# Kernel optimization log

Hardware: AMD Instinct MI355X
Metric: run time of the kernel (lower is better)

The kernel has to match this reference:

```python
import jax, jax.numpy as jnp
from jax import lax
import numpy as np

N = 200000
H = 64          # h
C = 2 * H       # 2h feature channels
L = 128         # voxel grid side
KV = 125        # 5^3 kernel volume
KEEP = KV // 2 + 1  # 63 offsets kept by mask type 'B' (incl. center)


def _build_kernel_map(coords):
    # coords: [N,3] int voxel coords, unique. Returns nidx [KEEP, N] int32, -1 if no neighbor.
    keys = (coords[:, 0].astype(np.int64) * L + coords[:, 1]) * L + coords[:, 2]
    order = np.argsort(keys)
    skeys = keys[order]
    nidx = np.full((KEEP, N), -1, dtype=np.int32)
    for k in range(KEEP):
        dx, dy, dz = k // 25 - 2, (k // 5) % 5 - 2, k % 5 - 2
        nc = coords + np.array([dx, dy, dz])
        inb = np.all((nc >= 0) & (nc < L), axis=1)
        qk = (nc[:, 0].astype(np.int64) * L + nc[:, 1]) * L + nc[:, 2]
        pos = np.searchsorted(skeys, qk)
        posc = np.minimum(pos, N - 1)
        found = inb & (skeys[posc] == qk)
        nidx[k] = np.where(found, order[posc].astype(np.int32), -1)
    return nidx


def setup_inputs() -> dict:
    key = jax.random.key(0)
    k1, k2, k3, k4, k5 = jax.random.split(key, 5)
    rng = np.random.default_rng(0)
    flat = rng.choice(L ** 3, size=N, replace=False)
    coords = np.stack(np.unravel_index(flat, (L, L, L)), axis=1).astype(np.int32)
    nidx = jnp.asarray(_build_kernel_map(coords))
    s = 0.05
    return {
        "x_feats": jax.random.normal(k1, (N, C), jnp.float32),
        "y_feats": jax.random.normal(k2, (N, C), jnp.float32),
        "Wa": jax.random.normal(k3, (C, H), jnp.float32) * s,
        "Wb": jax.random.normal(k4, (KV, H, H), jnp.float32) * s,
        "Wc": jax.random.normal(k5, (H, C), jnp.float32) * s,
        "nidx": nidx,
    }


def reference(x_feats, y_feats, Wa, Wb, Wc, nidx):
    # mask type 'B': zero kernel offsets >= KV//2 + 1
    mask = (jnp.arange(KV) < KEEP)[:, None, None].astype(Wb.dtype)
    Wb_kept = (Wb * mask)[:KEEP]  # [KEEP, H, H]; remaining offsets contribute 0

    def block(f):
        f = jax.nn.elu(f)
        f = f @ Wa                      # 1x1 conv 2h->h
        f = jax.nn.elu(f)
        # masked sparse 5^3 conv: gather-GEMM-accumulate over kernel offsets
        def body(acc, kw):
            idx, W = kw                 # idx [N], W [H,H]
            g = jnp.where((idx >= 0)[:, None], f[jnp.maximum(idx, 0)], 0.0)
            return acc + g @ W, None
        acc0 = jnp.zeros((f.shape[0], H), f.dtype)
        f, _ = lax.scan(body, acc0, (nidx, Wb_kept))
        f = jax.nn.elu(f)
        return f @ Wc                   # 1x1 conv h->2h

    out = x_feats + y_feats
    return x_feats + block(out)
```

## Files before the change

### kernel.cpp

```cpp
#include <hip/hip_runtime.h>
#include <cmath>

#define N_PTS 200000
#define HD 64
#define CD 128
#define KEEP 63

typedef __bf16 bf16;
typedef __bf16 bf16x4 __attribute__((ext_vector_type(4)));
typedef __bf16 bf16x8 __attribute__((ext_vector_type(8)));
typedef float f32x4 __attribute__((ext_vector_type(4)));
typedef float f32x16 __attribute__((ext_vector_type(16)));

__device__ __forceinline__ float elu_f(float v) {
    return v > 0.f ? v : __expf(v) - 1.f;
}

__global__ __launch_bounds__(256) void k_prep(const float* __restrict__ Wb,
                                              const float* __restrict__ Wc,
                                              const float* __restrict__ Wa,
                                              bf16* __restrict__ WbT,
                                              bf16* __restrict__ WcT,
                                              bf16* __restrict__ WaT,
                                              bf16* __restrict__ zp) {
    int idx = blockIdx.x * 256 + threadIdx.x;
    if (idx < KEEP * HD * HD) {
        int k = idx >> 12;
        int rem = idx & 4095;
        int o = rem >> 6, i = rem & 63;
        int dst = ((i >> 4) * 2 + (o >> 5)) * 512 +
                  (((i >> 3) & 1) * 32 + (o & 31)) * 8 + (i & 7);
        WbT[(k << 12) + dst] = (bf16)Wb[(k * HD + i) * HD + o];
        return;
    }
    int e = idx - KEEP * HD * HD;
    if (e < CD * HD) {
        int c = e >> 6, h = e & 63;
        WcT[e] = (bf16)Wc[h * CD + c];
        return;
    }
    e -= CD * HD;
    if (e < HD * CD) {
        int o = e >> 7, c = e & 127;
        int dst = ((c >> 4) * 2 + (o >> 5)) * 512 +
                  (((c >> 3) & 1) * 32 + (o & 31)) * 8 + (c & 7);
        WaT[dst] = (bf16)Wa[c * HD + o];
        return;
    }
    e -= HD * CD;
    if (e < 64) zp[e] = (bf16)0.f;
}

__global__ __launch_bounds__(256, 4) void k_stage1(const float* __restrict__ x,
                                                   const float* __restrict__ y,
                                                   const bf16* __restrict__ WaT,
                                                   bf16* __restrict__ f) {
    __shared__ bf16 pbuf[4][32 * 64];
    int tid = threadIdx.x;
    int wave = tid >> 6;
    int lane = tid & 63;
    int l31 = lane & 31;
    int half = lane >> 5;
    int pbase_w = blockIdx.x * 128 + wave * 32;
    int p = pbase_w + l31;
    int pc = p < N_PTS ? p : N_PTS - 1;

    const float* xr = x + (size_t)pc * CD;
    const float* yr = y + (size_t)pc * CD;

    f32x16 acc[2];
#pragma unroll
    for (int mt = 0; mt < 2; mt++)
#pragma unroll
        for (int r = 0; r < 16; r++) acc[mt][r] = 0.f;

    f32x4 xa[2], xb[2], ya[2], yb[2];
    {
        int c0 = half * 8;
        xa[0] = *(const f32x4*)(xr + c0);
        xb[0] = *(const f32x4*)(xr + c0 + 4);
        ya[0] = *(const f32x4*)(yr + c0);
        yb[0] = *(const f32x4*)(yr + c0 + 4);
    }
#pragma unroll
    for (int ks = 0; ks < 8; ks++) {
        int cur = ks & 1, nxt = cur ^ 1;
        bf16x8 a0 = *(const bf16x8*)(WaT + (ks * 2 + 0) * 512 + lane * 8);
        bf16x8 a1 = *(const bf16x8*)(WaT + (ks * 2 + 1) * 512 + lane * 8);
        __builtin_amdgcn_sched_barrier(0);
        if (ks < 7) {
            int c0 = half * 8 + (ks + 1) * 16;
            xa[nxt] = *(const f32x4*)(xr + c0);
            xb[nxt] = *(const f32x4*)(xr + c0 + 4);
            ya[nxt] = *(const f32x4*)(yr + c0);
            yb[nxt] = *(const f32x4*)(yr + c0 + 4);
        }
        bf16x8 bv;
#pragma unroll
        for (int jj = 0; jj < 4; jj++) {
            bv[jj]     = (bf16)elu_f(xa[cur][jj] + ya[cur][jj]);
            bv[4 + jj] = (bf16)elu_f(xb[cur][jj] + yb[cur][jj]);
        }
        acc[0] = __builtin_amdgcn_mfma_f32_32x32x16_bf16(a0, bv, acc[0], 0, 0, 0);
        acc[1] = __builtin_amdgcn_mfma_f32_32x32x16_bf16(a1, bv, acc[1], 0, 0, 0);
        __builtin_amdgcn_sched_barrier(0);
    }

    bf16* pb = pbuf[wave];
#pragma unroll
    for (int mt = 0; mt < 2; mt++) {
#pragma unroll
        for (int q = 0; q < 4; q++) {
            bf16x4 v;
#pragma unroll
            for (int jj = 0; jj < 4; jj++)
                v[jj] = (bf16)elu_f(acc[mt][q * 4 + jj]);
            int chunk = mt * 4 + q;
            *(bf16x4*)&pb[l31 * 64 + ((chunk ^ (l31 & 7)) * 8) + 4 * half] = v;
        }
    }
#pragma unroll
    for (int qq = 0; qq < 4; qq++) {
        int t = lane + 64 * qq;
        int row = t >> 3, ch = t & 7;
        int pos = ch ^ (row & 7);
        bf16x8 v = *(const bf16x8*)&pb[row * 64 + pos * 8];
        int pp = pbase_w + row;
        if (pp < N_PTS)
            *(bf16x8*)(f + (size_t)pp * HD + ch * 8) = v;
    }
}

struct BB { bf16x8 v[4]; };
struct AF { bf16x8 v[8]; };

__global__ __launch_bounds__(256, 2) void k_conv(const bf16* __restrict__ f,
                                                 const int* __restrict__ nidx,
                                                 const bf16* __restrict__ WbT,
                                                 const bf16* __restrict__ WcT,
                                                 const bf16* __restrict__ zp,
                                                 const float* __restrict__ x,
                                                 float* __restrict__ out) {
    __shared__ bf16 wcs[128 * 64];
    __shared__ bf16 pbuf[4 * 32 * 64];

    int tid = threadIdx.x;
    int wave = tid >> 6;
    int lane = tid & 63;
    int l31 = lane & 31;
    int half = lane >> 5;
    int pbase = blockIdx.x * 256 + wave * 64;
    int p0 = pbase + l31;
    int p1 = pbase + 32 + l31;

    f32x16 acc[2][2];
#pragma unroll
    for (int a = 0; a < 2; a++)
#pragma unroll
        for (int b = 0; b < 2; b++)
#pragma unroll
            for (int r = 0; r < 16; r++) acc[a][b][r] = 0.f;

#pragma unroll
    for (int L = tid; L < 1024; L += 256) {
        int c = L >> 3, ci = L & 7;
        bf16x8 v = *(const bf16x8*)&WcT[L * 8];
        *(bf16x8*)&wcs[c * 64 + ((ci ^ (c & 7)) * 8)] = v;
    }

    auto ldidx = [&](int k, int pp) -> int {
        return (k < KEEP && pp < N_PTS) ? nidx[(size_t)k * N_PTS + pp] : -1;
    };
    auto baddr = [&](int iv) -> const bf16* {
        return iv >= 0 ? f + (size_t)iv * HD + half * 8 : zp + half * 8;
    };
    auto gather = [&](BB& b, const bf16* a) {
#pragma unroll
        for (int ks = 0; ks < 4; ks++)
            b.v[ks] = *(const bf16x8*)(a + ks * 16);
    };
    auto loadA = [&](int k, AF& A) {
        const bf16* wk = WbT + ((size_t)k << 12);
#pragma unroll
        for (int fi = 0; fi < 8; fi++)
            A.v[fi] = *(const bf16x8*)(wk + fi * 512 + lane * 8);
    };
    auto mstep = [&](const AF& A, BB& q0, BB& q1) {
#pragma unroll
        for (int ks = 0; ks < 4; ks++) {
#pragma unroll
            for (int mt = 0; mt < 2; mt++) {
                acc[mt][0] = __builtin_amdgcn_mfma_f32_32x32x16_bf16(A.v[ks * 2 + mt], q0.v[ks], acc[mt][0], 0, 0, 0);
                acc[mt][1] = __builtin_amdgcn_mfma_f32_32x32x16_bf16(A.v[ks * 2 + mt], q1.v[ks], acc[mt][1], 0, 0, 0);
            }
        }
    };

    BB b0a, b0b, b1a, b1b, b2a, b2b;
    int i2a = ldidx(2, p0), i2b = ldidx(2, p1);
    int i0a = ldidx(3, p0), i0b = ldidx(3, p1);
    int i1a = ldidx(4, p0), i1b = ldidx(4, p1);
    {
        int ja = ldidx(0, p0), jb = ldidx(0, p1);
        int ka = ldidx(1, p0), kb = ldidx(1, p1);
        gather(b0a, baddr(ja)); gather(b0b, baddr(jb));
        gather(b1a, baddr(ka)); gather(b1b, baddr(kb));
    }

    AF Af;
    for (int j = 0; j < 20; j++) {
        int k = 3 * j;
        loadA(k, Af);
        __builtin_amdgcn_sched_barrier(0);
        gather(b2a, baddr(i2a)); gather(b2b, baddr(i2b));
        i2a = ldidx(k + 5, p0);  i2b = ldidx(k + 5, p1);
        mstep(Af, b0a, b0b);
        __builtin_amdgcn_sched_barrier(0);
        loadA(k + 1, Af);
        __builtin_amdgcn_sched_barrier(0);
        gather(b0a, baddr(i0a)); gather(b0b, baddr(i0b));
        i0a = ldidx(k + 6, p0);  i0b = ldidx(k + 6, p1);
        mstep(Af, b1a, b1b);
        __builtin_amdgcn_sched_barrier(0);
        loadA(k + 2, Af);
        __builtin_amdgcn_sched_barrier(0);
        gather(b1a, baddr(i1a)); gather(b1b, baddr(i1b));
        i1a = ldidx(k + 7, p0);  i1b = ldidx(k + 7, p1);
        mstep(Af, b2a, b2b);
        __builtin_amdgcn_sched_barrier(0);
    }
    loadA(60, Af);
    __builtin_amdgcn_sched_barrier(0);
    gather(b2a, baddr(i2a)); gather(b2b, baddr(i2b));
    mstep(Af, b0a, b0b);
    __builtin_amdgcn_sched_barrier(0);
    loadA(61, Af);
    __builtin_amdgcn_sched_barrier(0);
    mstep(Af, b1a, b1b);
    __builtin_amdgcn_sched_barrier(0);
    loadA(62, Af);
    __builtin_amdgcn_sched_barrier(0);
    mstep(Af, b2a, b2b);

    __syncthreads();

    bf16* pb = &pbuf[wave * 2048];
#pragma unroll
    for (int pt = 0; pt < 2; pt++) {
#pragma unroll
        for (int mt = 0; mt < 2; mt++) {
#pragma unroll
            for (int q = 0; q < 4; q++) {
                bf16x4 v;
#pragma unroll
                for (int jj = 0; jj < 4; jj++)
                    v[jj] = (bf16)elu_f(acc[mt][pt][q * 4 + jj]);
                int chunk = mt * 4 + q;
                *(bf16x4*)&pb[l31 * 64 + ((chunk ^ (l31 & 7)) * 8) + 4 * half] = v;
            }
        }
        bf16x8 pa[4];
#pragma unroll
        for (int ks = 0; ks < 4; ks++) {
            int ci = 2 * ks + half;
            pa[ks] = *(const bf16x8*)&pb[l31 * 64 + ((ci ^ (l31 & 7)) * 8)];
        }
#pragma unroll
        for (int ct = 0; ct < 4; ct++) {
            f32x16 o;
#pragma unroll
            for (int r = 0; r < 16; r++) o[r] = 0.f;
            int cc = ct * 32 + l31;
#pragma unroll
            for (int ks = 0; ks < 4; ks++) {
                int ci = 2 * ks + half;
                bf16x8 bw = *(const bf16x8*)&wcs[cc * 64 + ((ci ^ (cc & 7)) * 8)];
                o = __builtin_amdgcn_mfma_f32_32x32x16_bf16(pa[ks], bw, o, 0, 0, 0);
            }
            int prow_base = pbase + pt * 32 + 4 * half;
#pragma unroll
            for (int r = 0; r < 16; r++) {
                int prow = prow_base + (r & 3) + 8 * (r >> 2);
                if (prow < N_PTS) {
                    size_t off = (size_t)prow * CD + cc;
                    out[off] = x[off] + o[r];
                }
            }
        }
    }
}

extern "C" void kernel_launch(void* const* d_in, const int* in_sizes, int n_in,
                              void* d_out, int out_size, void* d_ws, size_t ws_size,
                              hipStream_t stream) {
    const float* x  = (const float*)d_in[0];
    const float* y  = (const float*)d_in[1];
    const float* Wa = (const float*)d_in[2];
    const float* Wb = (const float*)d_in[3];
    const float* Wc = (const float*)d_in[4];
    const int* nidx = (const int*)d_in[5];
    float* out = (float*)d_out;

    char* ws = (char*)d_ws;
    bf16* f   = (bf16*)ws;
    bf16* WbT = (bf16*)(ws + 25624576);
    bf16* WcT = (bf16*)(ws + 25624576 + 516096);
    bf16* WaT = (bf16*)(ws + 25624576 + 516096 + 16384);
    bf16* zp  = (bf16*)(ws + 25624576 + 516096 + 16384 + 16384);

    k_prep<<<1073, 256, 0, stream>>>(Wb, Wc, Wa, WbT, WcT, WaT, zp);
    k_stage1<<<1564, 256, 0, stream>>>(x, y, WaT, f);
    k_conv<<<782, 256, 0, stream>>>(f, nidx, WbT, WcT, zp, x, out);
}
```

Measured before the change: 551.8 us.

## Restructure sparse conv gather through per-wave LDS bounce with double-buffered weights

The conv kernel now gives each wave 32 points instead of 64. Neighbor rows are gathered with 8 lanes per row, so each 128-byte feature row is read contiguously. The gathered rows are staged in a swizzled per-wave LDS buffer and read back as MFMA operands. Weight fragments are double-buffered across kernel offsets, Wc is pre-laid-out in fragment order and read straight from global instead of LDS, and occupancy is raised to 4 blocks per CU. The aim is more coalesced gathers and better latency hiding, at the cost of reloading the weight fragments for every 32 points rather than every 64, plus extra LDS traffic. Stage1 prefetch is also deepened from 1 to 2 steps ahead.

```diff
diff --git a/kernel.cpp b/kernel.cpp
--- a/kernel.cpp
+++ b/kernel.cpp
@@ -20,7 +20,7 @@
                                               const float* __restrict__ Wc,
                                               const float* __restrict__ Wa,
                                               bf16* __restrict__ WbT,
-                                              bf16* __restrict__ WcT,
+                                              bf16* __restrict__ WcT2,
                                               bf16* __restrict__ WaT,
                                               bf16* __restrict__ zp) {
     int idx = blockIdx.x * 256 + threadIdx.x;
@@ -36,7 +36,9 @@
     int e = idx - KEEP * HD * HD;
     if (e < CD * HD) {
         int c = e >> 6, h = e & 63;
-        WcT[e] = (bf16)Wc[h * CD + c];
+        int dst = ((c >> 5) * 4 + (h >> 4)) * 512 +
+                  ((((h >> 3) & 1) * 32) + (c & 31)) * 8 + (h & 7);
+        WcT2[dst] = (bf16)Wc[h * CD + c];
         return;
     }
     e -= CD * HD;
@@ -74,22 +76,23 @@
 #pragma unroll
         for (int r = 0; r < 16; r++) acc[mt][r] = 0.f;
 
-    f32x4 xa[2], xb[2], ya[2], yb[2];
-    {
-        int c0 = half * 8;
-        xa[0] = *(const f32x4*)(xr + c0);
-        xb[0] = *(const f32x4*)(xr + c0 + 4);
-        ya[0] = *(const f32x4*)(yr + c0);
-        yb[0] = *(const f32x4*)(yr + c0 + 4);
+    f32x4 xa[3], xb[3], ya[3], yb[3];
+#pragma unroll
+    for (int pre = 0; pre < 2; pre++) {
+        int c0 = half * 8 + pre * 16;
+        xa[pre] = *(const f32x4*)(xr + c0);
+        xb[pre] = *(const f32x4*)(xr + c0 + 4);
+        ya[pre] = *(const f32x4*)(yr + c0);
+        yb[pre] = *(const f32x4*)(yr + c0 + 4);
     }
 #pragma unroll
     for (int ks = 0; ks < 8; ks++) {
-        int cur = ks & 1, nxt = cur ^ 1;
+        int cur = ks % 3, nxt = (ks + 2) % 3;
         bf16x8 a0 = *(const bf16x8*)(WaT + (ks * 2 + 0) * 512 + lane * 8);
         bf16x8 a1 = *(const bf16x8*)(WaT + (ks * 2 + 1) * 512 + lane * 8);
         __builtin_amdgcn_sched_barrier(0);
-        if (ks < 7) {
-            int c0 = half * 8 + (ks + 1) * 16;
+        if (ks < 6) {
+            int c0 = half * 8 + (ks + 2) * 16;
             xa[nxt] = *(const f32x4*)(xr + c0);
             xb[nxt] = *(const f32x4*)(xr + c0 + 4);
             ya[nxt] = *(const f32x4*)(yr + c0);
@@ -131,53 +134,53 @@
     }
 }
 
-struct BB { bf16x8 v[4]; };
+struct GR { bf16x8 v[4]; };
 struct AF { bf16x8 v[8]; };
 
-__global__ __launch_bounds__(256, 2) void k_conv(const bf16* __restrict__ f,
+__global__ __launch_bounds__(256, 4) void k_conv(const bf16* __restrict__ f,
                                                  const int* __restrict__ nidx,
                                                  const bf16* __restrict__ WbT,
-                                                 const bf16* __restrict__ WcT,
+                                                 const bf16* __restrict__ WcT2,
                                                  const bf16* __restrict__ zp,
                                                  const float* __restrict__ x,
                                                  float* __restrict__ out) {
-    __shared__ bf16 wcs[128 * 64];
-    __shared__ bf16 pbuf[4 * 32 * 64];
+    __shared__ bf16 bounce[4][32 * 64];
 
     int tid = threadIdx.x;
     int wave = tid >> 6;
     int lane = tid & 63;
     int l31 = lane & 31;
     int half = lane >> 5;
-    int pbase = blockIdx.x * 256 + wave * 64;
-    int p0 = pbase + l31;
-    int p1 = pbase + 32 + l31;
-
-    f32x16 acc[2][2];
-#pragma unroll
-    for (int a = 0; a < 2; a++)
-#pragma unroll
-        for (int b = 0; b < 2; b++)
-#pragma unroll
-            for (int r = 0; r < 16; r++) acc[a][b][r] = 0.f;
-
-#pragma unroll
-    for (int L = tid; L < 1024; L += 256) {
-        int c = L >> 3, ci = L & 7;
-        bf16x8 v = *(const bf16x8*)&WcT[L * 8];
-        *(bf16x8*)&wcs[c * 64 + ((ci ^ (c & 7)) * 8)] = v;
-    }
-
-    auto ldidx = [&](int k, int pp) -> int {
+    int g8 = lane >> 3;
+    int l7 = lane & 7;
+    int pbase = blockIdx.x * 128 + wave * 32;
+
+    bf16* pb = bounce[wave];
+
+    f32x16 acc[2];
+#pragma unroll
+    for (int mt = 0; mt < 2; mt++)
+#pragma unroll
+        for (int r = 0; r < 16; r++) acc[mt][r] = 0.f;
+
+    auto ldidx4 = [&](int k, int i) -> int {
+        int pp = pbase + i * 8 + g8;
         return (k < KEEP && pp < N_PTS) ? nidx[(size_t)k * N_PTS + pp] : -1;
     };
-    auto baddr = [&](int iv) -> const bf16* {
-        return iv >= 0 ? f + (size_t)iv * HD + half * 8 : zp + half * 8;
-    };
-    auto gather = [&](BB& b, const bf16* a) {
-#pragma unroll
-        for (int ks = 0; ks < 4; ks++)
-            b.v[ks] = *(const bf16x8*)(a + ks * 16);
+    auto gaddr = [&](int iv) -> const bf16* {
+        return iv >= 0 ? f + (size_t)iv * HD + l7 * 8 : zp + l7 * 8;
+    };
+    auto gather4 = [&](GR& g, const int (&iv)[4]) {
+#pragma unroll
+        for (int i = 0; i < 4; i++)
+            g.v[i] = *(const bf16x8*)gaddr(iv[i]);
+    };
+    auto dswrite = [&](const GR& g) {
+#pragma unroll
+        for (int i = 0; i < 4; i++) {
+            int pp = i * 8 + g8;
+            *(bf16x8*)&pb[pp * 64 + ((l7 ^ g8) * 8)] = g.v[i];
+        }
     };
     auto loadA = [&](int k, AF& A) {
         const bf16* wk = WbT + ((size_t)k << 12);
@@ -185,106 +188,100 @@
         for (int fi = 0; fi < 8; fi++)
             A.v[fi] = *(const bf16x8*)(wk + fi * 512 + lane * 8);
     };
-    auto mstep = [&](const AF& A, BB& q0, BB& q1) {
+    auto mfma8 = [&](const AF& a) {
 #pragma unroll
         for (int ks = 0; ks < 4; ks++) {
-#pragma unroll
-            for (int mt = 0; mt < 2; mt++) {
-                acc[mt][0] = __builtin_amdgcn_mfma_f32_32x32x16_bf16(A.v[ks * 2 + mt], q0.v[ks], acc[mt][0], 0, 0, 0);
-                acc[mt][1] = __builtin_amdgcn_mfma_f32_32x32x16_bf16(A.v[ks * 2 + mt], q1.v[ks], acc[mt][1], 0, 0, 0);
-            }
-        }
-    };
-
-    BB b0a, b0b, b1a, b1b, b2a, b2b;
-    int i2a = ldidx(2, p0), i2b = ldidx(2, p1);
-    int i0a = ldidx(3, p0), i0b = ldidx(3, p1);
-    int i1a = ldidx(4, p0), i1b = ldidx(4, p1);
+            int ci = ks * 2 + half;
+            bf16x8 fb = *(const bf16x8*)&pb[l31 * 64 + ((ci ^ (l31 & 7)) * 8)];
+            acc[0] = __builtin_amdgcn_mfma_f32_32x32x16_bf16(a.v[ks * 2 + 0], fb, acc[0], 0, 0, 0);
+            acc[1] = __builtin_amdgcn_mfma_f32_32x32x16_bf16(a.v[ks * 2 + 1], fb, acc[1], 0, 0, 0);
+        }
+    };
+    auto substep = [&](int k, AF& Aload, const AF& Ause, GR& gfill,
+                       const GR& gwrite, int (&slot)[4]) {
+        loadA(k + 1, Aload);
+        __builtin_amdgcn_sched_barrier(0);
+        gather4(gfill, slot);
+#pragma unroll
+        for (int i = 0; i < 4; i++) slot[i] = ldidx4(k + 6, i);
+        __builtin_amdgcn_sched_barrier(0);
+        mfma8(Ause);
+        __builtin_amdgcn_sched_barrier(0);
+        dswrite(gwrite);
+        __builtin_amdgcn_sched_barrier(0);
+    };
+
+    int s0[4], s1[4], s2[4], s3[4];
+#pragma unroll
+    for (int i = 0; i < 4; i++) s0[i] = ldidx4(2, i);
+#pragma unroll
+    for (int i = 0; i < 4; i++) s1[i] = ldidx4(3, i);
+#pragma unroll
+    for (int i = 0; i < 4; i++) s2[i] = ldidx4(4, i);
+#pragma unroll
+    for (int i = 0; i < 4; i++) s3[i] = ldidx4(5, i);
+    AF A0, A1;
+    GR ge, go;
     {
-        int ja = ldidx(0, p0), jb = ldidx(0, p1);
-        int ka = ldidx(1, p0), kb = ldidx(1, p1);
-        gather(b0a, baddr(ja)); gather(b0b, baddr(jb));
-        gather(b1a, baddr(ka)); gather(b1b, baddr(kb));
-    }
-
-    AF Af;
-    for (int j = 0; j < 20; j++) {
-        int k = 3 * j;
-        loadA(k, Af);
-        __builtin_amdgcn_sched_barrier(0);
-        gather(b2a, baddr(i2a)); gather(b2b, baddr(i2b));
-        i2a = ldidx(k + 5, p0);  i2b = ldidx(k + 5, p1);
-        mstep(Af, b0a, b0b);
-        __builtin_amdgcn_sched_barrier(0);
-        loadA(k + 1, Af);
-        __builtin_amdgcn_sched_barrier(0);
-        gather(b0a, baddr(i0a)); gather(b0b, baddr(i0b));
-        i0a = ldidx(k + 6, p0);  i0b = ldidx(k + 6, p1);
-        mstep(Af, b1a, b1b);
-        __builtin_amdgcn_sched_barrier(0);
-        loadA(k + 2, Af);
-        __builtin_amdgcn_sched_barrier(0);
-        gather(b1a, baddr(i1a)); gather(b1b, baddr(i1b));
-        i1a = ldidx(k + 7, p0);  i1b = ldidx(k + 7, p1);
-        mstep(Af, b2a, b2b);
-        __builtin_amdgcn_sched_barrier(0);
-    }
-    loadA(60, Af);
-    __builtin_amdgcn_sched_barrier(0);
-    gather(b2a, baddr(i2a)); gather(b2b, baddr(i2b));
-    mstep(Af, b0a, b0b);
-    __builtin_amdgcn_sched_barrier(0);
-    loadA(61, Af);
-    __builtin_amdgcn_sched_barrier(0);
-    mstep(Af, b1a, b1b);
-    __builtin_amdgcn_sched_barrier(0);
-    loadA(62, Af);
-    __builtin_amdgcn_sched_barrier(0);
-    mstep(Af, b2a, b2b);
-
-    __syncthreads();
-
-    bf16* pb = &pbuf[wave * 2048];
-#pragma unroll
-    for (int pt = 0; pt < 2; pt++) {
-#pragma unroll
-        for (int mt = 0; mt < 2; mt++) {
-#pragma unroll
-            for (int q = 0; q < 4; q++) {
-                bf16x4 v;
-#pragma unroll
-                for (int jj = 0; jj < 4; jj++)
-                    v[jj] = (bf16)elu_f(acc[mt][pt][q * 4 + jj]);
-                int chunk = mt * 4 + q;
-                *(bf16x4*)&pb[l31 * 64 + ((chunk ^ (l31 & 7)) * 8) + 4 * half] = v;
-            }
-        }
-        bf16x8 pa[4];
+        int i0[4], i1[4];
+#pragma unroll
+        for (int i = 0; i < 4; i++) i0[i] = ldidx4(0, i);
+#pragma unroll
+        for (int i = 0; i < 4; i++) i1[i] = ldidx4(1, i);
+        GR g0;
+        gather4(g0, i0);
+        gather4(go, i1);
+        dswrite(g0);
+        loadA(0, A0);
+    }
+
+    for (int j = 0; j < 15; j++) {
+        int k = 4 * j;
+        substep(k,     A1, A0, ge, go, s0);
+        substep(k + 1, A0, A1, go, ge, s1);
+        substep(k + 2, A1, A0, ge, go, s2);
+        substep(k + 3, A0, A1, go, ge, s3);
+    }
+    substep(60, A1, A0, ge, go, s0);
+    substep(61, A0, A1, go, ge, s1);
+    mfma8(A0);
+
+#pragma unroll
+    for (int mt = 0; mt < 2; mt++) {
+#pragma unroll
+        for (int q = 0; q < 4; q++) {
+            bf16x4 v;
+#pragma unroll
+            for (int jj = 0; jj < 4; jj++)
+                v[jj] = (bf16)elu_f(acc[mt][q * 4 + jj]);
+            int chunk = mt * 4 + q;
+            *(bf16x4*)&pb[l31 * 64 + ((chunk ^ (l31 & 7)) * 8) + 4 * half] = v;
+        }
+    }
+    bf16x8 pa[4];
+#pragma unroll
+    for (int ks = 0; ks < 4; ks++) {
+        int ci = 2 * ks + half;
+        pa[ks] = *(const bf16x8*)&pb[l31 * 64 + ((ci ^ (l31 & 7)) * 8)];
+    }
+#pragma unroll
+    for (int ct = 0; ct < 4; ct++) {
+        f32x16 o;
+#pragma unroll
+        for (int r = 0; r < 16; r++) o[r] = 0.f;
+        int cc = ct * 32 + l31;
 #pragma unroll
         for (int ks = 0; ks < 4; ks++) {
-            int ci = 2 * ks + half;
-            pa[ks] = *(const bf16x8*)&pb[l31 * 64 + ((ci ^ (l31 & 7)) * 8)];
-        }
-#pragma unroll
-        for (int ct = 0; ct < 4; ct++) {
-            f32x16 o;
-#pragma unroll
-            for (int r = 0; r < 16; r++) o[r] = 0.f;
-            int cc = ct * 32 + l31;
-#pragma unroll
-            for (int ks = 0; ks < 4; ks++) {
-                int ci = 2 * ks + half;
-                bf16x8 bw = *(const bf16x8*)&wcs[cc * 64 + ((ci ^ (cc & 7)) * 8)];
-                o = __builtin_amdgcn_mfma_f32_32x32x16_bf16(pa[ks], bw, o, 0, 0, 0);
-            }
-            int prow_base = pbase + pt * 32 + 4 * half;
-#pragma unroll
-            for (int r = 0; r < 16; r++) {
-                int prow = prow_base + (r & 3) + 8 * (r >> 2);
-                if (prow < N_PTS) {
-                    size_t off = (size_t)prow * CD + cc;
-                    out[off] = x[off] + o[r];
-                }
+            bf16x8 bw = *(const bf16x8*)(WcT2 + ((ct * 4 + ks) << 9) + lane * 8);
+            o = __builtin_amdgcn_mfma_f32_32x32x16_bf16(pa[ks], bw, o, 0, 0, 0);
+        }
+        int prow_base = pbase + 4 * half;
+#pragma unroll
+        for (int r = 0; r < 16; r++) {
+            int prow = prow_base + (r & 3) + 8 * (r >> 2);
+            if (prow < N_PTS) {
+                size_t off = (size_t)prow * CD + cc;
+                out[off] = x[off] + o[r];
             }
         }
     }
@@ -302,13 +299,13 @@
     float* out = (float*)d_out;
 
     char* ws = (char*)d_ws;
-    bf16* f   = (bf16*)ws;
-    bf16* WbT = (bf16*)(ws + 25624576);
-    bf16* WcT = (bf16*)(ws + 25624576 + 516096);
-    bf16* WaT = (bf16*)(ws + 25624576 + 516096 + 16384);
-    bf16* zp  = (bf16*)(ws + 25624576 + 516096 + 16384 + 16384);
-
-    k_prep<<<1073, 256, 0, stream>>>(Wb, Wc, Wa, WbT, WcT, WaT, zp);
-    k_stage1<<<1564, 256, 0, stream>>>(x, y, WaT, f);
-    k_conv<<<782, 256, 0, stream>>>(f, nidx, WbT, WcT, zp, x, out);
-}
+    bf16* f    = (bf16*)ws;
+    bf16* WbT  = (bf16*)(ws + 25624576);
+    bf16* WcT2 = (bf16*)(ws + 25624576 + 516096);
+    bf16* WaT  = (bf16*)(ws + 25624576 + 516096 + 16384);
+    bf16* zp   = (bf16*)(ws + 25624576 + 516096 + 16384 + 16384);
+
+    k_prep<<<1073, 256, 0, stream>>>(Wb, Wc, Wa, WbT, WcT2, WaT, zp);
+    k_stage1<<<1563, 256, 0, stream>>>(x, y, WaT, f);
+    k_conv<<<1563, 256, 0, stream>>>(f, nidx, WbT, WcT2, zp, x, out);
+}
```

Result: slower. 1.549 ms (+180.6%).
